# Optimization experiments

Hardware: AMD Instinct MI355X
Metric: run time of the kernel (lower is better)

The kernel has to match this reference:

```python
import jax, jax.numpy as jnp
import numpy as np
from math import sqrt

B, T, C, H = 4, 2048, 1024, 16
D = C // H  # head dim = 64


def setup_inputs() -> dict:
    key = jax.random.key(0)
    ks = jax.random.split(key, 9)
    s = 1.0 / sqrt(C)
    return {
        "x": jax.random.normal(ks[0], (B, T, C), dtype=jnp.float32),
        "Wk": jax.random.normal(ks[1], (C, C), dtype=jnp.float32) * s,
        "bk": jax.random.normal(ks[2], (C,), dtype=jnp.float32) * 0.01,
        "Wq": jax.random.normal(ks[3], (C, C), dtype=jnp.float32) * s,
        "bq": jax.random.normal(ks[4], (C,), dtype=jnp.float32) * 0.01,
        "Wv": jax.random.normal(ks[5], (C, C), dtype=jnp.float32) * s,
        "bv": jax.random.normal(ks[6], (C,), dtype=jnp.float32) * 0.01,
        "Wp": jax.random.normal(ks[7], (C, C), dtype=jnp.float32) * s,
        "bp": jax.random.normal(ks[8], (C,), dtype=jnp.float32) * 0.01,
    }


def reference(x, Wk, bk, Wq, bq, Wv, bv, Wp, bp):
    # Linear projections, split into heads: [B, H, T, D]
    def heads(y):
        return y.reshape(B, T, H, D).transpose(0, 2, 1, 3)

    k = heads(x @ Wk + bk)
    q = heads(x @ Wq + bq)
    v = heads(x @ Wv + bv)

    # scaled dot-product attention with causal mask (dropout p=0 -> identity)
    attn = jnp.einsum("bhtd,bhsd->bhts", q, k) / jnp.sqrt(jnp.float32(D))
    causal = jnp.tril(jnp.ones((T, T), dtype=bool))
    attn = jnp.where(causal[None, None], attn, -jnp.inf)
    attn = jax.nn.softmax(attn, axis=-1)

    y = jnp.einsum("bhts,bhsd->bhtd", attn, v)  # [B, H, T, D]
    y = y.transpose(0, 2, 1, 3).reshape(B, T, C)
    return y @ Wp + bp
```

## Files before the change

kernel.cpp:

```cpp
#include <hip/hip_runtime.h>
#include <hip/hip_bf16.h>
#include <math.h>


typedef short bf16x8 __attribute__((ext_vector_type(8)));
typedef float f32x4 __attribute__((ext_vector_type(4)));
typedef _Float16 f16x4 __attribute__((ext_vector_type(4)));

__device__ __forceinline__ short f2b(float f) {
    unsigned u = __float_as_uint(f);
    u = (u + 0x7fffu + ((u >> 16) & 1u)) >> 16;
    return (short)u;
}
__device__ __forceinline__ float b2f(short s) {
    return __uint_as_float(((unsigned)(unsigned short)s) << 16);
}

__global__ __launch_bounds__(256) void prep_kernel(const float* __restrict__ x, short* __restrict__ xb,
                                                   const float* W0, const float* W1,
                                                   const float* W2, const float* W3,
                                                   short* O0, short* O1, short* O2, short* O3) {
    int tid = threadIdx.x;
    if (blockIdx.x < 8192) {
        int idx = blockIdx.x * 256 + tid;
        float4 v = ((const float4*)x)[idx];
        short4 o;
        o.x = f2b(v.x); o.y = f2b(v.y); o.z = f2b(v.z); o.w = f2b(v.w);
        ((short4*)xb)[idx] = o;
        return;
    }
    int wid = blockIdx.x - 8192;
    const float* W; short* O;
    switch (wid >> 8) {
        case 0: W = W0; O = O0; break;
        case 1: W = W1; O = O1; break;
        case 2: W = W2; O = O2; break;
        default: W = W3; O = O3; break;
    }
    int rem = wid & 255;
    int n0 = (rem >> 4) * 64, k0 = (rem & 15) * 64;
    __shared__ __align__(16) float Ls[64 * 68];
    #pragma unroll
    for (int it = 0; it < 4; ++it) {
        int c = tid + it * 256;
        int r = c >> 4, off = (c & 15) * 4;
        *(float4*)&Ls[r * 68 + off] = *(const float4*)&W[(k0 + r) * 1024 + n0 + off];
    }
    __syncthreads();
    #pragma unroll
    for (int it = 0; it < 2; ++it) {
        int c = tid + it * 256;
        int n = c >> 3, koff = (c & 7) * 8;
        union { short s[8]; int4 v; } u;
        #pragma unroll
        for (int k = 0; k < 8; ++k) u.s[k] = f2b(Ls[(koff + k) * 68 + n]);
        *(int4*)&O[(n0 + n) * 1024 + k0 + koff] = u.v;
    }
}

template<int MODE>
__global__ __launch_bounds__(512, 2) void gemm8_kernel(const short* __restrict__ A,
                                                       const short* Bt0, const short* Bt1, const short* Bt2,
                                                       const float* b0, const float* b1, const float* b2,
                                                       float s0, float s1, float s2,
                                                       void* O0, void* O1, void* O2) {
    int z = blockIdx.z;
    const short* Bt   = (z == 0) ? Bt0 : (z == 1) ? Bt1 : Bt2;
    const float* bias = (z == 0) ? b0  : (z == 1) ? b1  : b2;
    float scl         = (z == 0) ? s0  : (z == 1) ? s1  : s2;
    void* Out         = (z == 0) ? O0  : (z == 1) ? O1  : O2;

    __shared__ __align__(16) short lds[73728];

    int tid = threadIdx.x;
    int w = tid >> 6, lane = tid & 63, quad = lane >> 4, l15 = lane & 15;
    int m0 = blockIdx.x * 128, n0 = blockIdx.y * 256;

    int srccol = ((lane & 3) * 8) ^ ((lane & 32) ? 16 : 0);
    const short* pA0 = A  + (m0 + w * 16 + (lane >> 2)) * 1024 + srccol;
    const short* pA1 = pA0 + 32;
    const short* pB0 = Bt + (n0 + (2 * w) * 16 + (lane >> 2)) * 1024 + srccol;
    const short* pB1 = pB0 + 32;
    const short* pB2 = pB0 + 16 * 1024;
    const short* pB3 = pB2 + 32;

    int dA = (w * 2) * 512;
    int dB = 24576 + (w * 4) * 512;

    int offR = l15 * 64 + ((quad * 16) ^ ((l15 & 8) << 2));
    int ma4 = (w >> 2) * 4;
    int nb2 = (w & 3) * 2;
    int jrow0 = nb2, jrow1 = nb2 + 1, jrow2 = nb2 + 8, jrow3 = nb2 + 9;
    const char* ldsb = (const char*)lds;

    f32x4 acc[4][4] = {};
    bf16x8 afA[4], bfA[4], afB[4], bfB[4];

#define STG(p, off) __builtin_amdgcn_global_load_lds( \
        (const __attribute__((address_space(1))) unsigned int*)(p), \
        (__attribute__((address_space(3))) unsigned int*)&lds[off], 16, 0, 0)
#define RD(base, row, kk) (*(const bf16x8*)(ldsb + (base) + ((row) * 2 + (kk)) * 1024 + offR))

    STG(pA0,      dA);                 STG(pA1,      dA + 512);
    STG(pB0,      dB);                 STG(pB1,      dB + 512);
    STG(pB2,      dB + 1024);          STG(pB3,      dB + 1536);
    STG(pA0 + 64, 8192 + dA);          STG(pA1 + 64, 8192 + dA + 512);
    STG(pB0 + 64, 16384 + dB);         STG(pB1 + 64, 16384 + dB + 512);
    STG(pB2 + 64, 16384 + dB + 1024);  STG(pB3 + 64, 16384 + dB + 1536);
    asm volatile("s_waitcnt vmcnt(6)" ::: "memory");
    __builtin_amdgcn_s_barrier();
    __builtin_amdgcn_sched_barrier(0);

    #pragma unroll
    for (int i = 0; i < 4; ++i) afA[i] = RD(0, ma4 + i, 0);
    bfA[0] = RD(49152, jrow0, 0); bfA[1] = RD(49152, jrow1, 0);
    bfA[2] = RD(49152, jrow2, 0); bfA[3] = RD(49152, jrow3, 0);

    #pragma unroll
    for (int t = 0; t < 16; ++t) {
        const int rs  = t % 3;
        const int rs1 = (t + 1) % 3;
        const int ss  = (t + 2) % 3;
        const int Ar  = rs * 16384;
        const int Br  = 49152 + rs * 32768;
        const int Ar1 = rs1 * 16384;
        const int Br1 = 49152 + rs1 * 32768;

        #pragma unroll
        for (int i = 0; i < 4; ++i) afB[i] = RD(Ar, ma4 + i, 1);
        bfB[0] = RD(Br, jrow0, 1); bfB[1] = RD(Br, jrow1, 1);
        bfB[2] = RD(Br, jrow2, 1); bfB[3] = RD(Br, jrow3, 1);
        if (t + 2 < 16) {
            STG(pA0 + (t + 2) * 64, ss * 8192 + dA);
            STG(pA1 + (t + 2) * 64, ss * 8192 + dA + 512);
            STG(pB0 + (t + 2) * 64, ss * 16384 + dB);
        }
        asm volatile("s_waitcnt lgkmcnt(8)" ::: "memory");
        __builtin_amdgcn_sched_barrier(0);
        __builtin_amdgcn_s_setprio(1);
        #pragma unroll
        for (int i = 0; i < 4; ++i)
            #pragma unroll
            for (int j = 0; j < 4; ++j)
                acc[i][j] = __builtin_amdgcn_mfma_f32_16x16x32_bf16(afA[i], bfA[j], acc[i][j], 0, 0, 0);
        __builtin_amdgcn_s_setprio(0);
        if (t < 14) {
            asm volatile("s_waitcnt vmcnt(3)" ::: "memory");
        } else if (t == 14) {
            asm volatile("s_waitcnt vmcnt(0)" ::: "memory");
        }
        __builtin_amdgcn_s_barrier();
        __builtin_amdgcn_sched_barrier(0);

        if (t < 15) {
            #pragma unroll
            for (int i = 0; i < 4; ++i) afA[i] = RD(Ar1, ma4 + i, 0);
            bfA[0] = RD(Br1, jrow0, 0); bfA[1] = RD(Br1, jrow1, 0);
            bfA[2] = RD(Br1, jrow2, 0); bfA[3] = RD(Br1, jrow3, 0);
        }
        if (t + 2 < 16) {
            STG(pB1 + (t + 2) * 64, ss * 16384 + dB + 512);
            STG(pB2 + (t + 2) * 64, ss * 16384 + dB + 1024);
            STG(pB3 + (t + 2) * 64, ss * 16384 + dB + 1536);
        }
        if (t < 15) {
            asm volatile("s_waitcnt lgkmcnt(8)" ::: "memory");
        } else {
            asm volatile("s_waitcnt lgkmcnt(0)" ::: "memory");
        }
        __builtin_amdgcn_sched_barrier(0);
        __builtin_amdgcn_s_setprio(1);
        #pragma unroll
        for (int i = 0; i < 4; ++i)
            #pragma unroll
            for (int j = 0; j < 4; ++j)
                acc[i][j] = __builtin_amdgcn_mfma_f32_16x16x32_bf16(afB[i], bfB[j], acc[i][j], 0, 0, 0);
        __builtin_amdgcn_s_setprio(0);
        if (t < 15) {
            __builtin_amdgcn_s_barrier();
            __builtin_amdgcn_sched_barrier(0);
        }
    }
#undef STG
#undef RD

    int mrow = m0 + (w >> 2) * 64;
    int ncol = n0 + (w & 3) * 32;
    #pragma unroll
    for (int i = 0; i < 4; ++i) {
        #pragma unroll
        for (int j = 0; j < 4; ++j) {
            int gn = ncol + (j >> 1) * 128 + (j & 1) * 16 + l15;
            float bv = bias[gn];
            if (MODE == 0 && z == 2) {
                int gm0 = mrow + i * 16 + quad * 4;
                int b = gm0 >> 11, tt = gm0 & 2047, h = gn >> 6, d = gn & 63;
                f16x4 hv;
                #pragma unroll
                for (int r = 0; r < 4; ++r) hv[r] = (_Float16)((acc[i][j][r] + bv) * scl);
                *(f16x4*)&((_Float16*)Out)[((b * 16 + h) * 64 + d) * 2048 + tt] = hv;
            } else {
                #pragma unroll
                for (int r = 0; r < 4; ++r) {
                    int gm = mrow + i * 16 + quad * 4 + r;
                    float v = (acc[i][j][r] + bv) * scl;
                    if (MODE == 0) {
                        int b = gm >> 11, tt = gm & 2047, h = gn >> 6, d = gn & 63;
                        ((short*)Out)[(((b * 16 + h) * 2048) + tt) * 64 + d] = f2b(v);
                    } else {
                        ((float*)Out)[gm * 1024 + gn] = v;
                    }
                }
            }
        }
    }
}

__global__ __launch_bounds__(256, 2) void attn_kernel(const short* __restrict__ Q,
                                                      const short* __restrict__ K,
                                                      const _Float16* __restrict__ Vt,
                                                      short* __restrict__ Y) {
    __shared__ __align__(16) short    Ks[2][128 * 64];
    __shared__ __align__(16) _Float16 Vs[2][64 * 128];

    int tid = threadIdx.x;
    int w = tid >> 6, lane = tid & 63, quad = lane >> 4, l15 = lane & 15;
    int idx = blockIdx.x;
    int qi = 15 - (idx >> 6);
    int bh = idx & 63;

    const short* Qh = Q + bh * 2048 * 64;
    const short* Kh = K + bh * 2048 * 64;
    const _Float16* Vh = Vt + bh * 64 * 2048;

    bf16x8 qf[2][2];
    #pragma unroll
    for (int i = 0; i < 2; ++i)
        #pragma unroll
        for (int kh = 0; kh < 2; ++kh) {
            int t = qi * 128 + w * 32 + i * 16 + l15;
            qf[i][kh] = *(const bf16x8*)&Qh[t * 64 + kh * 32 + quad * 8];
        }

    int krow = lane >> 3;
    int kchunk = ((lane & 7) ^ krow) * 8;
    int vrow = lane >> 4;
    int vchunk = ((lane & 15) ^ (w * 4 + vrow)) * 8;

    int t7 = l15 & 7;
    int kf0_off = ((quad ^ t7) * 8);
    int kf1_off = (((quad + 4) ^ t7) * 8);
    int vsub = (quad & 1) * 4;
    int vchi = quad >> 1;

    f32x4 o[2][4] = {};
    float lsum[2] = {0.f, 0.f};

    asm volatile("s_waitcnt vmcnt(0)" ::: "memory");
    __builtin_amdgcn_sched_barrier(0);

#define ASTAGE(si_, buf_) do { \
    const short* Kt_ = Kh + (si_) * 128 * 64; \
    const _Float16* Vt_ = Vh + (si_) * 128; \
    _Pragma("unroll") \
    for (int it = 0; it < 4; ++it) { \
        int kr0 = it * 32 + w * 8; \
        __builtin_amdgcn_global_load_lds( \
            (const __attribute__((address_space(1))) unsigned int*)&Kt_[(kr0 + krow) * 64 + kchunk], \
            (__attribute__((address_space(3))) unsigned int*)&Ks[buf_][kr0 * 64], 16, 0, 0); \
        int vr0 = it * 16 + w * 4; \
        __builtin_amdgcn_global_load_lds( \
            (const __attribute__((address_space(1))) unsigned int*)&Vt_[(vr0 + vrow) * 2048 + vchunk], \
            (__attribute__((address_space(3))) unsigned int*)&Vs[buf_][vr0 * 128], 16, 0, 0); \
    } } while (0)

    ASTAGE(0, 0);

    for (int si = 0; si <= qi; ++si) {
        int buf = si & 1;
        if (si < qi) {
            ASTAGE(si + 1, buf ^ 1);
            asm volatile("s_waitcnt vmcnt(8)" ::: "memory");
        } else {
            asm volatile("s_waitcnt vmcnt(0)" ::: "memory");
        }
        __builtin_amdgcn_s_barrier();
        __builtin_amdgcn_sched_barrier(0);

        const short* Ksb = Ks[buf];
        const _Float16* Vsb = Vs[buf];
        bool diag = (si == qi);

        #pragma unroll
        for (int j = 0; j < 8; ++j) {
            int trow = (j * 16 + l15) * 64;
            bf16x8 kf0 = *(const bf16x8*)&Ksb[trow + kf0_off];
            bf16x8 kf1 = *(const bf16x8*)&Ksb[trow + kf1_off];
            f16x4 pfv[2];
            #pragma unroll
            for (int i = 0; i < 2; ++i) {
                f32x4 a = {};
                a = __builtin_amdgcn_mfma_f32_16x16x32_bf16(kf0, qf[i][0], a, 0, 0, 0);
                a = __builtin_amdgcn_mfma_f32_16x16x32_bf16(kf1, qf[i][1], a, 0, 0, 0);
                if (diag) {
                    int qrel = w * 32 + i * 16 + l15;
                    #pragma unroll
                    for (int r = 0; r < 4; ++r)
                        if (j * 16 + quad * 4 + r > qrel) a[r] = -1e30f;
                }
                float p0 = __builtin_amdgcn_exp2f(a[0]);
                float p1 = __builtin_amdgcn_exp2f(a[1]);
                float p2 = __builtin_amdgcn_exp2f(a[2]);
                float p3 = __builtin_amdgcn_exp2f(a[3]);
                lsum[i] += (p0 + p1) + (p2 + p3);
                pfv[i][0] = (_Float16)p0;
                pfv[i][1] = (_Float16)p1;
                pfv[i][2] = (_Float16)p2;
                pfv[i][3] = (_Float16)p3;
            }
            int vc = (j * 2 + vchi);
            #pragma unroll
            for (int mt = 0; mt < 4; ++mt) {
                int d = mt * 16 + l15;
                f16x4 vf = *(const f16x4*)&Vsb[d * 128 + ((vc ^ l15) * 8) + vsub];
                o[0][mt] = __builtin_amdgcn_mfma_f32_16x16x16f16(vf, pfv[0], o[0][mt], 0, 0, 0);
                o[1][mt] = __builtin_amdgcn_mfma_f32_16x16x16f16(vf, pfv[1], o[1][mt], 0, 0, 0);
            }
        }

        asm volatile("s_waitcnt lgkmcnt(0)" ::: "memory");
        __builtin_amdgcn_s_barrier();
        __builtin_amdgcn_sched_barrier(0);
    }
#undef ASTAGE

    int b = bh >> 4, h = bh & 15;
    #pragma unroll
    for (int i = 0; i < 2; ++i) {
        float l = lsum[i];
        l += __shfl_xor(l, 16);
        l += __shfl_xor(l, 32);
        float rinv = 1.0f / l;
        int q = qi * 128 + w * 32 + i * 16 + l15;
        short* yrow = &Y[(b * 2048 + q) * 1024 + h * 64];
        #pragma unroll
        for (int mt = 0; mt < 4; ++mt) {
            short4 s4;
            s4.x = f2b(o[i][mt][0] * rinv);
            s4.y = f2b(o[i][mt][1] * rinv);
            s4.z = f2b(o[i][mt][2] * rinv);
            s4.w = f2b(o[i][mt][3] * rinv);
            *(short4*)&yrow[mt * 16 + quad * 4] = s4;
        }
    }
}

extern "C" void kernel_launch(void* const* d_in, const int* in_sizes, int n_in,
                              void* d_out, int out_size, void* d_ws, size_t ws_size,
                              hipStream_t stream) {
    const float* x  = (const float*)d_in[0];
    const float* Wk = (const float*)d_in[1];
    const float* bk = (const float*)d_in[2];
    const float* Wq = (const float*)d_in[3];
    const float* bq = (const float*)d_in[4];
    const float* Wv = (const float*)d_in[5];
    const float* bv = (const float*)d_in[6];
    const float* Wp = (const float*)d_in[7];
    const float* bp = (const float*)d_in[8];

    char* ws = (char*)d_ws;
    short*     xb  = (short*)(ws + 0);
    short*     Wqt = (short*)(ws + 16777216);
    short*     Wkt = (short*)(ws + 18874368);
    short*     Wvt = (short*)(ws + 20971520);
    short*     Wpt = (short*)(ws + 23068672);
    short*     Qb  = (short*)(ws + 25165824);
    short*     Kb  = (short*)(ws + 41943040);
    _Float16*  Vtb = (_Float16*)(ws + 75497472);
    short*     Yb  = (short*)(ws + 92274688);

    prep_kernel<<<9216, 256, 0, stream>>>(x, xb, Wq, Wk, Wv, Wp, Wqt, Wkt, Wvt, Wpt);
    gemm8_kernel<0><<<dim3(64, 4, 3), 512, 0, stream>>>(xb, Wqt, Wkt, Wvt, bq, bk, bv,
                                                        0.18033688011112042f , 1.0f, 1.0f,
                                                        (void*)Qb, (void*)Kb, (void*)Vtb);
    attn_kernel<<<1024, 256, 0, stream>>>(Qb, Kb, Vtb, Yb);
    gemm8_kernel<1><<<dim3(64, 4, 1), 512, 0, stream>>>(Yb, Wpt, nullptr, nullptr,
                                                        bp, nullptr, nullptr,
                                                        1.0f, 1.0f, 1.0f,
                                                        (void*)d_out, nullptr, nullptr);
}
```

Baseline: 237.1 us.

## Single-buffer V tile in attention to allow three blocks per CU

The V shared-memory tile goes from double to single buffering, cutting LDS use from 64KB to 48KB per block, and launch bounds rise to 3 blocks per CU. K is still double-buffered and prefetched at the start of each step. V for the next step is loaded only after a barrier at the end of the current step, so its latency is no longer hidden within the block. The bet is that higher occupancy hides that latency across blocks, at the cost of tighter register limits and possible spills.

After: 238.7 us. No clear change (+0.7%).

```diff
diff --git a/kernel.cpp b/kernel.cpp
--- a/kernel.cpp
+++ b/kernel.cpp
@@ -216,12 +216,12 @@
     }
 }
 
-__global__ __launch_bounds__(256, 2) void attn_kernel(const short* __restrict__ Q,
+__global__ __launch_bounds__(256, 3) void attn_kernel(const short* __restrict__ Q,
                                                       const short* __restrict__ K,
                                                       const _Float16* __restrict__ Vt,
                                                       short* __restrict__ Y) {
     __shared__ __align__(16) short    Ks[2][128 * 64];
-    __shared__ __align__(16) _Float16 Vs[2][64 * 128];
+    __shared__ __align__(16) _Float16 Vs[64 * 128];
 
     int tid = threadIdx.x;
     int w = tid >> 6, lane = tid & 63, quad = lane >> 4, l15 = lane & 15;
@@ -256,39 +256,36 @@
     f32x4 o[2][4] = {};
     float lsum[2] = {0.f, 0.f};
 
-    asm volatile("s_waitcnt vmcnt(0)" ::: "memory");
-    __builtin_amdgcn_sched_barrier(0);
-
-#define ASTAGE(si_, buf_) do { \
+#define STGK(si_, buf_) do { \
     const short* Kt_ = Kh + (si_) * 128 * 64; \
-    const _Float16* Vt_ = Vh + (si_) * 128; \
     _Pragma("unroll") \
     for (int it = 0; it < 4; ++it) { \
         int kr0 = it * 32 + w * 8; \
         __builtin_amdgcn_global_load_lds( \
             (const __attribute__((address_space(1))) unsigned int*)&Kt_[(kr0 + krow) * 64 + kchunk], \
             (__attribute__((address_space(3))) unsigned int*)&Ks[buf_][kr0 * 64], 16, 0, 0); \
+    } } while (0)
+#define STGV(si_) do { \
+    const _Float16* Vp_ = Vh + (si_) * 128; \
+    _Pragma("unroll") \
+    for (int it = 0; it < 4; ++it) { \
         int vr0 = it * 16 + w * 4; \
         __builtin_amdgcn_global_load_lds( \
-            (const __attribute__((address_space(1))) unsigned int*)&Vt_[(vr0 + vrow) * 2048 + vchunk], \
-            (__attribute__((address_space(3))) unsigned int*)&Vs[buf_][vr0 * 128], 16, 0, 0); \
+            (const __attribute__((address_space(1))) unsigned int*)&Vp_[(vr0 + vrow) * 2048 + vchunk], \
+            (__attribute__((address_space(3))) unsigned int*)&Vs[vr0 * 128], 16, 0, 0); \
     } } while (0)
 
-    ASTAGE(0, 0);
+    STGK(0, 0);
+    STGV(0);
 
     for (int si = 0; si <= qi; ++si) {
-        int buf = si & 1;
-        if (si < qi) {
-            ASTAGE(si + 1, buf ^ 1);
-            asm volatile("s_waitcnt vmcnt(8)" ::: "memory");
-        } else {
-            asm volatile("s_waitcnt vmcnt(0)" ::: "memory");
-        }
+        asm volatile("s_waitcnt vmcnt(0)" ::: "memory");
         __builtin_amdgcn_s_barrier();
         __builtin_amdgcn_sched_barrier(0);
 
-        const short* Ksb = Ks[buf];
-        const _Float16* Vsb = Vs[buf];
+        if (si < qi) STGK(si + 1, (si + 1) & 1);
+
+        const short* Ksb = Ks[si & 1];
         bool diag = (si == qi);
 
         #pragma unroll
@@ -322,17 +319,21 @@
             #pragma unroll
             for (int mt = 0; mt < 4; ++mt) {
                 int d = mt * 16 + l15;
-                f16x4 vf = *(const f16x4*)&Vsb[d * 128 + ((vc ^ l15) * 8) + vsub];
+                f16x4 vf = *(const f16x4*)&Vs[d * 128 + ((vc ^ l15) * 8) + vsub];
                 o[0][mt] = __builtin_amdgcn_mfma_f32_16x16x16f16(vf, pfv[0], o[0][mt], 0, 0, 0);
                 o[1][mt] = __builtin_amdgcn_mfma_f32_16x16x16f16(vf, pfv[1], o[1][mt], 0, 0, 0);
             }
         }
 
-        asm volatile("s_waitcnt lgkmcnt(0)" ::: "memory");
-        __builtin_amdgcn_s_barrier();
-        __builtin_amdgcn_sched_barrier(0);
-    }
-#undef ASTAGE
+        if (si < qi) {
+            asm volatile("s_waitcnt lgkmcnt(0)" ::: "memory");
+            __builtin_amdgcn_s_barrier();
+            __builtin_amdgcn_sched_barrier(0);
+            STGV(si + 1);
+        }
+    }
+#undef STGK
+#undef STGV
 
     int b = bh >> 4, h = bh & 15;
     #pragma unroll
```
